# Kernel optimization log

Hardware: AMD Instinct MI355X
Metric: run time of the kernel (lower is better)

## Reference

```python
import jax, jax.numpy as jnp
import numpy as np

B, T = 256, 256          # batch, encoder sequence length
XD, SD, AD = 512, 512, 512  # xDim, sDim, attDim (emdDim == attDim)
YD = 6625                # vocab size (tgt_embedding has YD+1 rows)


def setup_inputs() -> dict:
    key = jax.random.key(0)
    ks = jax.random.split(key, 18)
    f32 = jnp.float32
    std = 0.02

    def rnd(k, shape, s=std):
        return jax.random.normal(k, shape, f32) * s

    return {
        "x": jax.random.normal(ks[0], (B, T, XD), f32),
        "sPrev": jax.random.normal(ks[1], (1, B, SD), f32),
        "yPrev": jax.random.randint(ks[2], (B,), 0, YD),
        # AttentionUnit params
        "xe_w": rnd(ks[3], (AD, XD)), "xe_b": rnd(ks[4], (AD,)),
        "se_w": rnd(ks[5], (AD, SD)), "se_b": rnd(ks[6], (AD,)),
        "we_w": rnd(ks[7], (1, AD)), "we_b": rnd(ks[8], (1,)),
        # target embedding (init std=0.01 per source)
        "emb": jax.random.normal(ks[9], (YD + 1, AD), f32) * 0.01,
        # GRUCell params: input = xDim + emdDim, hidden = sDim
        "gru_w_ih": rnd(ks[10], (3 * SD, XD + AD)),
        "gru_w_hh": rnd(ks[11], (3 * SD, SD)),
        "gru_b_ih": rnd(ks[12], (3 * SD,)),
        "gru_b_hh": rnd(ks[13], (3 * SD,)),
        # output projection (bias init to zeros per source)
        "fc_w": rnd(ks[14], (YD, SD)),
        "fc_b": jnp.zeros((YD,), f32),
    }


def reference(x, sPrev, yPrev, xe_w, xe_b, se_w, se_b, we_w, we_b, emb,
              gru_w_ih, gru_w_hh, gru_b_ih, gru_b_hh, fc_w, fc_b):
    s = sPrev[0]  # [B, SD]
    # additive attention: tanh(sProj + xProj) -> scalar score per (b, t)
    xProj = jnp.einsum('btx,ax->bta', x, xe_w) + xe_b          # [B, T, AD]
    sProj = s @ se_w.T + se_b                                  # [B, AD]
    scores = jnp.tanh(xProj + sProj[:, None, :]) @ we_w[0] + we_b[0]  # [B, T]
    alpha = jax.nn.softmax(scores, axis=1)                     # [B, T]
    context = jnp.einsum('bt,btx->bx', alpha, x)               # [B, XD]

    yProj = emb[yPrev]                                         # [B, AD]
    cc = jnp.concatenate([yProj, context], axis=1)             # [B, AD+XD]

    # torch GRUCell gates
    gi = cc @ gru_w_ih.T + gru_b_ih                            # [B, 3*SD]
    gh = s @ gru_w_hh.T + gru_b_hh                             # [B, 3*SD]
    i_r, i_z, i_n = jnp.split(gi, 3, axis=1)
    h_r, h_z, h_n = jnp.split(gh, 3, axis=1)
    r = jax.nn.sigmoid(i_r + h_r)
    z = jax.nn.sigmoid(i_z + h_z)
    n = jnp.tanh(i_n + r * h_n)
    h = (1.0 - z) * n + z * s                                  # [B, SD]

    logits = h @ fc_w.T + fc_b                                 # [B, YD]
    return logits, h
```

## Files before the change

### kernel.cpp

```cpp
#include <hip/hip_runtime.h>
#include <stdint.h>
#include <stddef.h>

typedef __attribute__((ext_vector_type(4))) float f32x4;
typedef __attribute__((ext_vector_type(2))) float f32x2;
typedef __attribute__((ext_vector_type(8))) __bf16 bf16x8;

#define DEVI static __device__ __forceinline__

DEVI f32x4 mfma16(bf16x8 a, bf16x8 b, f32x4 c){
  return __builtin_amdgcn_mfma_f32_16x16x32_bf16(a, b, c, 0, 0, 0);
}

DEVI bf16x8 cvt8(f32x4 a, f32x4 b){
  bf16x8 o;
  o[0]=(__bf16)a[0]; o[1]=(__bf16)a[1]; o[2]=(__bf16)a[2]; o[3]=(__bf16)a[3];
  o[4]=(__bf16)b[0]; o[5]=(__bf16)b[1]; o[6]=(__bf16)b[2]; o[7]=(__bf16)b[3];
  return o;
}

DEVI float fast_tanh(float x){ return 1.f - 2.f/(__expf(2.f*x)+1.f); }
DEVI float sigm(float x){ return 1.f/(1.f+__expf(-x)); }

__global__ __launch_bounds__(256) void cvt_xew(const float* __restrict__ xe_w,
                                               __bf16* __restrict__ wswz){
  int g = blockIdx.x*256 + threadIdx.x;
  int tile = g >> 9;
  int s = g & 511;
  int nt = tile >> 3, kt = tile & 7;
  int r = s >> 3, cp = s & 7;
  int cg = cp ^ (r & 7);
  const float* src = xe_w + (size_t)(nt*64 + r)*512 + kt*64 + cg*8;
  f32x4 a = *(const f32x4*)src;
  f32x4 b = *(const f32x4*)(src + 4);
  *(bf16x8*)(wswz + (size_t)g*8) = cvt8(a, b);
}

__global__ __launch_bounds__(256) void gemm_bt(
    const float* __restrict__ A, const float* __restrict__ W,
    const float* __restrict__ bias0, const float* __restrict__ bias1,
    float* __restrict__ Cf, int K, int Nreal, int ldc)
{
  const int tid  = threadIdx.x;
  const int lane = tid & 63;
  const int wid  = tid >> 6;
  const int wr = wid >> 1, wc = wid & 1;
  const int n0 = blockIdx.x * 64;
  const int m0 = blockIdx.y * 64;

  __shared__ __bf16 As[64*64];
  __shared__ __bf16 Wt[64*64];

  f32x4 acc[2][2] = {};

  const int nkt = K >> 6;
  for (int kt = 0; kt < nkt; ++kt){
    #pragma unroll
    for (int ss = 0; ss < 2; ++ss){
      int s  = ss*256 + tid;
      int r  = s >> 3;
      int cp = s & 7;
      int cg = cp ^ (r & 7);
      {
        const float* g = A + (size_t)(m0 + r)*K + kt*64 + cg*8;
        f32x4 v0 = *(const f32x4*)g;
        f32x4 v1 = *(const f32x4*)(g + 4);
        *(bf16x8*)(As + (size_t)s*8) = cvt8(v0, v1);
      }
      {
        int rw = n0 + r;
        if (rw >= Nreal) rw = Nreal - 1;
        const float* g = W + (size_t)rw*K + kt*64 + cg*8;
        f32x4 v0 = *(const f32x4*)g;
        f32x4 v1 = *(const f32x4*)(g + 4);
        *(bf16x8*)(Wt + (size_t)s*8) = cvt8(v0, v1);
      }
    }
    __syncthreads();
    #pragma unroll
    for (int kk = 0; kk < 2; ++kk){
      bf16x8 af[2], wf[2];
      #pragma unroll
      for (int mi = 0; mi < 2; ++mi){
        int r  = wr*32 + mi*16 + (lane & 15);
        int c  = kk*4 + (lane >> 4);
        int cs = c ^ (r & 7);
        af[mi] = *(const bf16x8*)(As + (size_t)r*64 + cs*8);
      }
      #pragma unroll
      for (int ni = 0; ni < 2; ++ni){
        int r  = wc*32 + ni*16 + (lane & 15);
        int c  = kk*4 + (lane >> 4);
        int cs = c ^ (r & 7);
        wf[ni] = *(const bf16x8*)(Wt + (size_t)r*64 + cs*8);
      }
      #pragma unroll
      for (int mi = 0; mi < 2; ++mi)
        #pragma unroll
        for (int ni = 0; ni < 2; ++ni)
          acc[mi][ni] = mfma16(af[mi], wf[ni], acc[mi][ni]);
    }
    __syncthreads();
  }

  #pragma unroll
  for (int mi = 0; mi < 2; ++mi){
    #pragma unroll
    for (int ni = 0; ni < 2; ++ni){
      int rbase = m0 + wr*32 + mi*16 + (lane >> 4)*4;
      int col   = n0 + wc*32 + ni*16 + (lane & 15);
      if (col < Nreal){
        float bb = 0.f;
        if (bias0) bb += bias0[col];
        if (bias1) bb += bias1[col];
        #pragma unroll
        for (int r4 = 0; r4 < 4; ++r4){
          Cf[(size_t)(rbase + r4)*ldc + col] = acc[mi][ni][r4] + bb;
        }
      }
    }
  }
}

__global__ __launch_bounds__(256) void attn_scores(
    const float* __restrict__ x, const __bf16* __restrict__ wswz,
    const float* __restrict__ sProjPlus, const float* __restrict__ we_w,
    float* __restrict__ scores)
{
  const int tid  = threadIdx.x;
  const int lane = tid & 63;
  const int wid  = tid >> 6;
  const int wr = wid >> 1, wc = wid & 1;
  const int m0 = blockIdx.x * 64;
  const int b  = m0 >> 8;

  __shared__ __bf16 Xs[64*512];
  __shared__ __bf16 Ws[64*64];
  __shared__ float  sc[2][64];

  if (tid < 64){ sc[0][tid] = 0.f; sc[1][tid] = 0.f; }

  #pragma unroll 4
  for (int i = 0; i < 16; ++i){
    int s  = i*256 + tid;
    int r  = s >> 6;
    int cp = s & 63;
    int cg = cp ^ (r & 7);
    const float* g = x + (size_t)(m0 + r)*512 + cg*8;
    f32x4 v0 = *(const f32x4*)g;
    f32x4 v1 = *(const f32x4*)(g + 4);
    *(bf16x8*)(Xs + (size_t)s*8) = cvt8(v0, v1);
  }
  __syncthreads();

  #pragma unroll 1
  for (int nt = 0; nt < 8; ++nt){
    f32x4 acc[2][2] = {};
    #pragma unroll 1
    for (int kt = 0; kt < 8; ++kt){
      const bf16x8* wsrc = (const bf16x8*)(wswz + (size_t)(nt*8 + kt)*4096);
      bf16x8 w0 = wsrc[tid];
      bf16x8 w1 = wsrc[tid + 256];
      ((bf16x8*)Ws)[tid]       = w0;
      ((bf16x8*)Ws)[tid + 256] = w1;
      __syncthreads();
      #pragma unroll
      for (int kk = 0; kk < 2; ++kk){
        bf16x8 af[2], wf[2];
        #pragma unroll
        for (int mi = 0; mi < 2; ++mi){
          int r  = wr*32 + mi*16 + (lane & 15);
          int c  = kt*8 + kk*4 + (lane >> 4);
          int cs = c ^ (r & 7);
          af[mi] = *(const bf16x8*)(Xs + (size_t)r*512 + cs*8);
        }
        #pragma unroll
        for (int ni = 0; ni < 2; ++ni){
          int r  = wc*32 + ni*16 + (lane & 15);
          int c  = kk*4 + (lane >> 4);
          int cs = c ^ (r & 7);
          wf[ni] = *(const bf16x8*)(Ws + (size_t)r*64 + cs*8);
        }
        #pragma unroll
        for (int mi = 0; mi < 2; ++mi)
          #pragma unroll
          for (int ni = 0; ni < 2; ++ni)
            acc[mi][ni] = mfma16(af[mi], wf[ni], acc[mi][ni]);
      }
      __syncthreads();
    }
    float part[2][4] = {};
    #pragma unroll
    for (int ni = 0; ni < 2; ++ni){
      int col  = nt*64 + wc*32 + ni*16 + (lane & 15);
      float sp = sProjPlus[b*512 + col];
      float wv = we_w[col];
      #pragma unroll
      for (int mi = 0; mi < 2; ++mi)
        #pragma unroll
        for (int r4 = 0; r4 < 4; ++r4){
          float t = fast_tanh(acc[mi][ni][r4] + sp);
          part[mi][r4] += t * wv;
        }
    }
    #pragma unroll
    for (int mi = 0; mi < 2; ++mi)
      #pragma unroll
      for (int r4 = 0; r4 < 4; ++r4){
        float v = part[mi][r4];
        v += __shfl_xor(v, 1);
        v += __shfl_xor(v, 2);
        v += __shfl_xor(v, 4);
        v += __shfl_xor(v, 8);
        if ((lane & 15) == 0){
          int row = wr*32 + mi*16 + (lane >> 4)*4 + r4;
          sc[wc][row] += v;
        }
      }
  }
  __syncthreads();
  if (tid < 64) scores[m0 + tid] = sc[0][tid] + sc[1][tid];
}

__global__ __launch_bounds__(256) void softmax_k(const float* __restrict__ scores,
                                                 float* __restrict__ alpha){
  int b = blockIdx.x, t = threadIdx.x;
  __shared__ float red[256];
  float v = scores[b*256 + t];
  red[t] = v; __syncthreads();
  for (int o = 128; o > 0; o >>= 1){
    if (t < o) red[t] = fmaxf(red[t], red[t+o]);
    __syncthreads();
  }
  float m = red[0]; __syncthreads();
  float e = __expf(v - m);
  red[t] = e; __syncthreads();
  for (int o = 128; o > 0; o >>= 1){
    if (t < o) red[t] += red[t+o];
    __syncthreads();
  }
  alpha[b*256 + t] = e / red[0];
}

__global__ __launch_bounds__(256) void context_cc(
    const float* __restrict__ x, const float* __restrict__ alpha,
    const float* __restrict__ emb, const int* __restrict__ yPrev,
    float* __restrict__ cc)
{
  int b = blockIdx.x, t = threadIdx.x;
  __shared__ float al[256];
  al[t] = alpha[b*256 + t];
  __syncthreads();
  f32x2 acc = {0.f, 0.f};
  const f32x2* xb = (const f32x2*)(x + (size_t)b*256*512) + t;
  #pragma unroll 4
  for (int i = 0; i < 256; ++i){
    f32x2 v = xb[(size_t)i*256];
    acc.x += al[i]*v.x;
    acc.y += al[i]*v.y;
  }
  int yp = yPrev[b];
  f32x2 e2 = ((const f32x2*)(emb + (size_t)yp*512))[t];
  f32x2* ccb = (f32x2*)(cc + (size_t)b*1024);
  ccb[t]       = e2;
  ccb[256 + t] = acc;
}

__global__ __launch_bounds__(256) void gates_k(
    const float* __restrict__ gi, const float* __restrict__ gh,
    const float* __restrict__ s, float* __restrict__ h_out)
{
  int idx = blockIdx.x*256 + threadIdx.x;
  int b = idx >> 9, j = idx & 511;
  const float* gib = gi + (size_t)b*1536;
  const float* ghb = gh + (size_t)b*1536;
  float r  = sigm(gib[j]        + ghb[j]);
  float z  = sigm(gib[512 + j]  + ghb[512 + j]);
  float nv = fast_tanh(gib[1024 + j] + r*ghb[1024 + j]);
  float sv = s[idx];
  float h  = (1.f - z)*nv + z*sv;
  h_out[idx] = h;
}

extern "C" void kernel_launch(void* const* d_in, const int* in_sizes, int n_in,
                              void* d_out, int out_size, void* d_ws, size_t ws_size,
                              hipStream_t stream)
{
  const float* x     = (const float*)d_in[0];
  const float* sPrev = (const float*)d_in[1];
  const int*   yPrev = (const int*)d_in[2];
  const float* xe_w  = (const float*)d_in[3];
  const float* xe_b  = (const float*)d_in[4];
  const float* se_w  = (const float*)d_in[5];
  const float* se_b  = (const float*)d_in[6];
  const float* we_w  = (const float*)d_in[7];
  const float* emb   = (const float*)d_in[9];
  const float* w_ih  = (const float*)d_in[10];
  const float* w_hh  = (const float*)d_in[11];
  const float* b_ih  = (const float*)d_in[12];
  const float* b_hh  = (const float*)d_in[13];
  const float* fc_w  = (const float*)d_in[14];
  const float* fc_b  = (const float*)d_in[15];

  char* ws = (char*)d_ws;
  __bf16* wswz  = (__bf16*)(ws);
  float* sProjP = (float*)(ws + 524288);
  float* gh     = (float*)(ws + 1048576);
  float* scores = (float*)(ws + 2621440);
  float* alpha  = (float*)(ws + 2883584);
  float* cc     = (float*)(ws + 3145728);
  float* gi     = (float*)(ws + 4194304);

  float* logits_out = (float*)d_out;
  float* h_out      = logits_out + (size_t)256*6625;

  cvt_xew<<<128, 256, 0, stream>>>(xe_w, wswz);
  gemm_bt<<<dim3(8,4),  256, 0, stream>>>(sPrev, se_w, se_b, xe_b, sProjP, 512, 512, 512);
  gemm_bt<<<dim3(24,4), 256, 0, stream>>>(sPrev, w_hh, b_hh, nullptr, gh, 512, 1536, 1536);
  attn_scores<<<1024, 256, 0, stream>>>(x, wswz, sProjP, we_w, scores);
  softmax_k<<<256, 256, 0, stream>>>(scores, alpha);
  context_cc<<<256, 256, 0, stream>>>(x, alpha, emb, yPrev, cc);
  gemm_bt<<<dim3(24,4), 256, 0, stream>>>(cc, w_ih, b_ih, nullptr, gi, 1024, 1536, 1536);
  gates_k<<<512, 256, 0, stream>>>(gi, gh, sPrev, h_out);
  gemm_bt<<<dim3(104,4), 256, 0, stream>>>(h_out, fc_w, fc_b, nullptr, logits_out, 512, 6625, 6625);
}
```

Baseline: 448.0 us.

## Retile attention and fc GEMMs to 128x128, fuse small GEMMs, split context reduction

The attention-score kernel is restructured into a 128x128 tiled GEMM grid split over four column blocks. It writes four partial scores per row, and softmax sums them. The two small sPrev GEMMs are fused into one launch. The output fc GEMM moves to a new 128x128 tile kernel. context_cc uses 512 threads and splits the T reduction in two halves. The intent is better MFMA reuse, more parallelism, and fewer launches, at the cost of fewer blocks for the fc GEMM and extra partial-score traffic.

After: 392.6 us. 1.14x faster.

```diff
diff --git a/kernel.cpp b/kernel.cpp
--- a/kernel.cpp
+++ b/kernel.cpp
@@ -36,23 +36,17 @@
   *(bf16x8*)(wswz + (size_t)g*8) = cvt8(a, b);
 }
 
-__global__ __launch_bounds__(256) void gemm_bt(
-    const float* __restrict__ A, const float* __restrict__ W,
-    const float* __restrict__ bias0, const float* __restrict__ bias1,
-    float* __restrict__ Cf, int K, int Nreal, int ldc)
+DEVI void gemm64_core(const float* __restrict__ A, const float* __restrict__ W,
+                      const float* __restrict__ bias0, const float* __restrict__ bias1,
+                      float* __restrict__ Cf, int K, int Nreal, int ldc,
+                      int m0, int n0, __bf16* As, __bf16* Wt)
 {
   const int tid  = threadIdx.x;
   const int lane = tid & 63;
   const int wid  = tid >> 6;
   const int wr = wid >> 1, wc = wid & 1;
-  const int n0 = blockIdx.x * 64;
-  const int m0 = blockIdx.y * 64;
-
-  __shared__ __bf16 As[64*64];
-  __shared__ __bf16 Wt[64*64];
 
   f32x4 acc[2][2] = {};
-
   const int nkt = K >> 6;
   for (int kt = 0; kt < nkt; ++kt){
     #pragma unroll
@@ -114,119 +108,228 @@
         if (bias0) bb += bias0[col];
         if (bias1) bb += bias1[col];
         #pragma unroll
-        for (int r4 = 0; r4 < 4; ++r4){
+        for (int r4 = 0; r4 < 4; ++r4)
           Cf[(size_t)(rbase + r4)*ldc + col] = acc[mi][ni][r4] + bb;
-        }
-      }
-    }
-  }
-}
-
-__global__ __launch_bounds__(256) void attn_scores(
-    const float* __restrict__ x, const __bf16* __restrict__ wswz,
-    const float* __restrict__ sProjPlus, const float* __restrict__ we_w,
-    float* __restrict__ scores)
+      }
+    }
+  }
+}
+
+__global__ __launch_bounds__(256) void gemm_bt(
+    const float* __restrict__ A, const float* __restrict__ W,
+    const float* __restrict__ bias0, const float* __restrict__ bias1,
+    float* __restrict__ Cf, int K, int Nreal, int ldc)
+{
+  __shared__ __bf16 As[64*64];
+  __shared__ __bf16 Wt[64*64];
+  gemm64_core(A, W, bias0, bias1, Cf, K, Nreal, ldc,
+              blockIdx.y*64, blockIdx.x*64, As, Wt);
+}
+
+__global__ __launch_bounds__(256) void gemm_small_fused(
+    const float* __restrict__ s,
+    const float* __restrict__ se_w, const float* __restrict__ se_b,
+    const float* __restrict__ xe_b, float* __restrict__ sProjP,
+    const float* __restrict__ w_hh, const float* __restrict__ b_hh,
+    float* __restrict__ gh)
+{
+  __shared__ __bf16 As[64*64];
+  __shared__ __bf16 Wt[64*64];
+  int bid = blockIdx.x;
+  if (bid < 32){
+    gemm64_core(s, se_w, se_b, xe_b, sProjP, 512, 512, 512,
+                (bid >> 3)*64, (bid & 7)*64, As, Wt);
+  } else {
+    int b2 = bid - 32;
+    gemm64_core(s, w_hh, b_hh, nullptr, gh, 512, 1536, 1536,
+                (b2 / 24)*64, (b2 % 24)*64, As, Wt);
+  }
+}
+
+__global__ __launch_bounds__(256) void gemm128_bt(
+    const float* __restrict__ A, const float* __restrict__ W,
+    const float* __restrict__ bias, float* __restrict__ C,
+    int K, int Nreal, int ldc)
 {
   const int tid  = threadIdx.x;
   const int lane = tid & 63;
   const int wid  = tid >> 6;
   const int wr = wid >> 1, wc = wid & 1;
-  const int m0 = blockIdx.x * 64;
+  const int n0 = blockIdx.x * 128;
+  const int m0 = blockIdx.y * 128;
+
+  __shared__ __bf16 As[128*64];
+  __shared__ __bf16 Bs[128*64];
+
+  f32x4 acc[4][4] = {};
+  const int nkt = K >> 6;
+  for (int kt = 0; kt < nkt; ++kt){
+    #pragma unroll
+    for (int i = 0; i < 4; ++i){
+      int s  = i*256 + tid;
+      int r  = s >> 3;
+      int cp = s & 7;
+      int cg = cp ^ (r & 7);
+      {
+        const float* g = A + (size_t)(m0 + r)*K + kt*64 + cg*8;
+        f32x4 v0 = *(const f32x4*)g;
+        f32x4 v1 = *(const f32x4*)(g + 4);
+        *(bf16x8*)(As + (size_t)s*8) = cvt8(v0, v1);
+      }
+      {
+        int rw = n0 + r;
+        if (rw >= Nreal) rw = Nreal - 1;
+        const float* g = W + (size_t)rw*K + kt*64 + cg*8;
+        f32x4 v0 = *(const f32x4*)g;
+        f32x4 v1 = *(const f32x4*)(g + 4);
+        *(bf16x8*)(Bs + (size_t)s*8) = cvt8(v0, v1);
+      }
+    }
+    __syncthreads();
+    #pragma unroll
+    for (int kk = 0; kk < 2; ++kk){
+      bf16x8 af[4], bfr[4];
+      #pragma unroll
+      for (int mi = 0; mi < 4; ++mi){
+        int r  = wr*64 + mi*16 + (lane & 15);
+        int c  = kk*4 + (lane >> 4);
+        int cs = c ^ (r & 7);
+        af[mi] = *(const bf16x8*)(As + (size_t)r*64 + cs*8);
+      }
+      #pragma unroll
+      for (int ni = 0; ni < 4; ++ni){
+        int r  = wc*64 + ni*16 + (lane & 15);
+        int c  = kk*4 + (lane >> 4);
+        int cs = c ^ (r & 7);
+        bfr[ni] = *(const bf16x8*)(Bs + (size_t)r*64 + cs*8);
+      }
+      #pragma unroll
+      for (int mi = 0; mi < 4; ++mi)
+        #pragma unroll
+        for (int ni = 0; ni < 4; ++ni)
+          acc[mi][ni] = mfma16(af[mi], bfr[ni], acc[mi][ni]);
+    }
+    __syncthreads();
+  }
+
+  #pragma unroll
+  for (int mi = 0; mi < 4; ++mi){
+    #pragma unroll
+    for (int ni = 0; ni < 4; ++ni){
+      int rbase = m0 + wr*64 + mi*16 + (lane >> 4)*4;
+      int col   = n0 + wc*64 + ni*16 + (lane & 15);
+      if (col < Nreal){
+        float bb = bias ? bias[col] : 0.f;
+        #pragma unroll
+        for (int r4 = 0; r4 < 4; ++r4)
+          C[(size_t)(rbase + r4)*ldc + col] = acc[mi][ni][r4] + bb;
+      }
+    }
+  }
+}
+
+__global__ __launch_bounds__(256) void attn_scores2(
+    const float* __restrict__ x, const __bf16* __restrict__ wswz,
+    const float* __restrict__ sProjPlus, const float* __restrict__ we_w,
+    float* __restrict__ scores4)
+{
+  const int tid  = threadIdx.x;
+  const int lane = tid & 63;
+  const int wid  = tid >> 6;
+  const int wr = wid >> 1, wc = wid & 1;
+  const int nb = blockIdx.x;
+  const int m0 = blockIdx.y * 128;
   const int b  = m0 >> 8;
 
-  __shared__ __bf16 Xs[64*512];
-  __shared__ __bf16 Ws[64*64];
-  __shared__ float  sc[2][64];
-
-  if (tid < 64){ sc[0][tid] = 0.f; sc[1][tid] = 0.f; }
-
-  #pragma unroll 4
-  for (int i = 0; i < 16; ++i){
-    int s  = i*256 + tid;
-    int r  = s >> 6;
-    int cp = s & 63;
-    int cg = cp ^ (r & 7);
-    const float* g = x + (size_t)(m0 + r)*512 + cg*8;
-    f32x4 v0 = *(const f32x4*)g;
-    f32x4 v1 = *(const f32x4*)(g + 4);
-    *(bf16x8*)(Xs + (size_t)s*8) = cvt8(v0, v1);
-  }
+  __shared__ __bf16 As[128*64];
+  __shared__ __bf16 Bs[128*64];
+  __shared__ float  sc[2][128];
+
+  f32x4 acc[4][4] = {};
+  #pragma unroll 1
+  for (int kt = 0; kt < 8; ++kt){
+    #pragma unroll
+    for (int i = 0; i < 4; ++i){
+      int s  = i*256 + tid;
+      int r  = s >> 3;
+      int cp = s & 7;
+      int cg = cp ^ (r & 7);
+      const float* g = x + (size_t)(m0 + r)*512 + kt*64 + cg*8;
+      f32x4 v0 = *(const f32x4*)g;
+      f32x4 v1 = *(const f32x4*)(g + 4);
+      *(bf16x8*)(As + (size_t)s*8) = cvt8(v0, v1);
+    }
+    {
+      const bf16x8* t0 = (const bf16x8*)(wswz + (size_t)((2*nb)*8   + kt)*4096);
+      const bf16x8* t1 = (const bf16x8*)(wswz + (size_t)((2*nb+1)*8 + kt)*4096);
+      bf16x8* bs = (bf16x8*)Bs;
+      bs[tid]       = t0[tid];
+      bs[tid + 256] = t0[tid + 256];
+      bs[tid + 512] = t1[tid];
+      bs[tid + 768] = t1[tid + 256];
+    }
+    __syncthreads();
+    #pragma unroll
+    for (int kk = 0; kk < 2; ++kk){
+      bf16x8 af[4], bfr[4];
+      #pragma unroll
+      for (int mi = 0; mi < 4; ++mi){
+        int r  = wr*64 + mi*16 + (lane & 15);
+        int c  = kk*4 + (lane >> 4);
+        int cs = c ^ (r & 7);
+        af[mi] = *(const bf16x8*)(As + (size_t)r*64 + cs*8);
+      }
+      #pragma unroll
+      for (int ni = 0; ni < 4; ++ni){
+        int r  = wc*64 + ni*16 + (lane & 15);
+        int c  = kk*4 + (lane >> 4);
+        int cs = c ^ (r & 7);
+        bfr[ni] = *(const bf16x8*)(Bs + (size_t)r*64 + cs*8);
+      }
+      #pragma unroll
+      for (int mi = 0; mi < 4; ++mi)
+        #pragma unroll
+        for (int ni = 0; ni < 4; ++ni)
+          acc[mi][ni] = mfma16(af[mi], bfr[ni], acc[mi][ni]);
+    }
+    __syncthreads();
+  }
+
+  float part[4][4] = {};
+  #pragma unroll
+  for (int ni = 0; ni < 4; ++ni){
+    int col  = nb*128 + wc*64 + ni*16 + (lane & 15);
+    float sp = sProjPlus[b*512 + col];
+    float wv = we_w[col];
+    #pragma unroll
+    for (int mi = 0; mi < 4; ++mi)
+      #pragma unroll
+      for (int r4 = 0; r4 < 4; ++r4)
+        part[mi][r4] += fast_tanh(acc[mi][ni][r4] + sp) * wv;
+  }
+  #pragma unroll
+  for (int mi = 0; mi < 4; ++mi)
+    #pragma unroll
+    for (int r4 = 0; r4 < 4; ++r4){
+      float v = part[mi][r4];
+      v += __shfl_xor(v, 1);
+      v += __shfl_xor(v, 2);
+      v += __shfl_xor(v, 4);
+      v += __shfl_xor(v, 8);
+      if ((lane & 15) == 0)
+        sc[wc][wr*64 + mi*16 + (lane >> 4)*4 + r4] = v;
+    }
   __syncthreads();
-
-  #pragma unroll 1
-  for (int nt = 0; nt < 8; ++nt){
-    f32x4 acc[2][2] = {};
-    #pragma unroll 1
-    for (int kt = 0; kt < 8; ++kt){
-      const bf16x8* wsrc = (const bf16x8*)(wswz + (size_t)(nt*8 + kt)*4096);
-      bf16x8 w0 = wsrc[tid];
-      bf16x8 w1 = wsrc[tid + 256];
-      ((bf16x8*)Ws)[tid]       = w0;
-      ((bf16x8*)Ws)[tid + 256] = w1;
-      __syncthreads();
-      #pragma unroll
-      for (int kk = 0; kk < 2; ++kk){
-        bf16x8 af[2], wf[2];
-        #pragma unroll
-        for (int mi = 0; mi < 2; ++mi){
-          int r  = wr*32 + mi*16 + (lane & 15);
-          int c  = kt*8 + kk*4 + (lane >> 4);
-          int cs = c ^ (r & 7);
-          af[mi] = *(const bf16x8*)(Xs + (size_t)r*512 + cs*8);
-        }
-        #pragma unroll
-        for (int ni = 0; ni < 2; ++ni){
-          int r  = wc*32 + ni*16 + (lane & 15);
-          int c  = kk*4 + (lane >> 4);
-          int cs = c ^ (r & 7);
-          wf[ni] = *(const bf16x8*)(Ws + (size_t)r*64 + cs*8);
-        }
-        #pragma unroll
-        for (int mi = 0; mi < 2; ++mi)
-          #pragma unroll
-          for (int ni = 0; ni < 2; ++ni)
-            acc[mi][ni] = mfma16(af[mi], wf[ni], acc[mi][ni]);
-      }
-      __syncthreads();
-    }
-    float part[2][4] = {};
-    #pragma unroll
-    for (int ni = 0; ni < 2; ++ni){
-      int col  = nt*64 + wc*32 + ni*16 + (lane & 15);
-      float sp = sProjPlus[b*512 + col];
-      float wv = we_w[col];
-      #pragma unroll
-      for (int mi = 0; mi < 2; ++mi)
-        #pragma unroll
-        for (int r4 = 0; r4 < 4; ++r4){
-          float t = fast_tanh(acc[mi][ni][r4] + sp);
-          part[mi][r4] += t * wv;
-        }
-    }
-    #pragma unroll
-    for (int mi = 0; mi < 2; ++mi)
-      #pragma unroll
-      for (int r4 = 0; r4 < 4; ++r4){
-        float v = part[mi][r4];
-        v += __shfl_xor(v, 1);
-        v += __shfl_xor(v, 2);
-        v += __shfl_xor(v, 4);
-        v += __shfl_xor(v, 8);
-        if ((lane & 15) == 0){
-          int row = wr*32 + mi*16 + (lane >> 4)*4 + r4;
-          sc[wc][row] += v;
-        }
-      }
-  }
-  __syncthreads();
-  if (tid < 64) scores[m0 + tid] = sc[0][tid] + sc[1][tid];
-}
-
-__global__ __launch_bounds__(256) void softmax_k(const float* __restrict__ scores,
+  if (tid < 128)
+    scores4[(size_t)(m0 + tid)*4 + nb] = sc[0][tid] + sc[1][tid];
+}
+
+__global__ __launch_bounds__(256) void softmax_k(const float* __restrict__ scores4,
                                                  float* __restrict__ alpha){
   int b = blockIdx.x, t = threadIdx.x;
   __shared__ float red[256];
-  float v = scores[b*256 + t];
+  f32x4 s4 = *(const f32x4*)(scores4 + (size_t)(b*256 + t)*4);
+  float v = (s4[0] + s4[1]) + (s4[2] + s4[3]);
   red[t] = v; __syncthreads();
   for (int o = 128; o > 0; o >>= 1){
     if (t < o) red[t] = fmaxf(red[t], red[t+o]);
@@ -242,28 +345,34 @@
   alpha[b*256 + t] = e / red[0];
 }
 
-__global__ __launch_bounds__(256) void context_cc(
+__global__ __launch_bounds__(512) void context_cc(
     const float* __restrict__ x, const float* __restrict__ alpha,
     const float* __restrict__ emb, const int* __restrict__ yPrev,
     float* __restrict__ cc)
 {
-  int b = blockIdx.x, t = threadIdx.x;
+  int b = blockIdx.x, th = threadIdx.x;
   __shared__ float al[256];
-  al[t] = alpha[b*256 + t];
+  __shared__ float px[512], py[512];
+  if (th < 256) al[th] = alpha[b*256 + th];
   __syncthreads();
+  int cp = th & 255, half = th >> 8;
   f32x2 acc = {0.f, 0.f};
-  const f32x2* xb = (const f32x2*)(x + (size_t)b*256*512) + t;
+  const f32x2* xb = (const f32x2*)(x + (size_t)b*131072) + cp;
   #pragma unroll 4
-  for (int i = 0; i < 256; ++i){
+  for (int i = half*128; i < half*128 + 128; ++i){
     f32x2 v = xb[(size_t)i*256];
     acc.x += al[i]*v.x;
     acc.y += al[i]*v.y;
   }
-  int yp = yPrev[b];
-  f32x2 e2 = ((const f32x2*)(emb + (size_t)yp*512))[t];
-  f32x2* ccb = (f32x2*)(cc + (size_t)b*1024);
-  ccb[t]       = e2;
-  ccb[256 + t] = acc;
+  px[th] = acc.x; py[th] = acc.y;
+  __syncthreads();
+  if (th < 256){
+    f32x2 e2 = ((const f32x2*)(emb + (size_t)yPrev[b]*512))[th];
+    f32x2* ccb = (f32x2*)(cc + (size_t)b*1024);
+    ccb[th] = e2;
+    f32x2 c2 = { px[th] + px[th+256], py[th] + py[th+256] };
+    ccb[256 + th] = c2;
+  }
 }
 
 __global__ __launch_bounds__(256) void gates_k(
@@ -303,24 +412,24 @@
   const float* fc_b  = (const float*)d_in[15];
 
   char* ws = (char*)d_ws;
-  __bf16* wswz  = (__bf16*)(ws);
-  float* sProjP = (float*)(ws + 524288);
-  float* gh     = (float*)(ws + 1048576);
-  float* scores = (float*)(ws + 2621440);
-  float* alpha  = (float*)(ws + 2883584);
-  float* cc     = (float*)(ws + 3145728);
-  float* gi     = (float*)(ws + 4194304);
+  __bf16* wswz   = (__bf16*)(ws);
+  float* sProjP  = (float*)(ws + 524288);
+  float* gh      = (float*)(ws + 1048576);
+  float* scores4 = (float*)(ws + 2621440);
+  float* alpha   = (float*)(ws + 3670016);
+  float* cc      = (float*)(ws + 2621440);
+  float* gi      = (float*)(ws + 3932160);
 
   float* logits_out = (float*)d_out;
   float* h_out      = logits_out + (size_t)256*6625;
 
   cvt_xew<<<128, 256, 0, stream>>>(xe_w, wswz);
-  gemm_bt<<<dim3(8,4),  256, 0, stream>>>(sPrev, se_w, se_b, xe_b, sProjP, 512, 512, 512);
-  gemm_bt<<<dim3(24,4), 256, 0, stream>>>(sPrev, w_hh, b_hh, nullptr, gh, 512, 1536, 1536);
-  attn_scores<<<1024, 256, 0, stream>>>(x, wswz, sProjP, we_w, scores);
-  softmax_k<<<256, 256, 0, stream>>>(scores, alpha);
-  context_cc<<<256, 256, 0, stream>>>(x, alpha, emb, yPrev, cc);
+  gemm_small_fused<<<128, 256, 0, stream>>>(sPrev, se_w, se_b, xe_b, sProjP,
+                                            w_hh, b_hh, gh);
+  attn_scores2<<<dim3(4, 512), 256, 0, stream>>>(x, wswz, sProjP, we_w, scores4);
+  softmax_k<<<256, 256, 0, stream>>>(scores4, alpha);
+  context_cc<<<256, 512, 0, stream>>>(x, alpha, emb, yPrev, cc);
   gemm_bt<<<dim3(24,4), 256, 0, stream>>>(cc, w_ih, b_ih, nullptr, gi, 1024, 1536, 1536);
   gates_k<<<512, 256, 0, stream>>>(gi, gh, sPrev, h_out);
-  gemm_bt<<<dim3(104,4), 256, 0, stream>>>(h_out, fc_w, fc_b, nullptr, logits_out, 512, 6625, 6625);
-}
+  gemm128_bt<<<dim3(52,2), 256, 0, stream>>>(h_out, fc_w, fc_b, logits_out, 512, 6625, 6625);
+}
```
